# Kernel optimization log

Hardware: AMD Instinct MI355X
Metric: run time of the kernel (lower is better)

## Reference

```python
import jax, jax.numpy as jnp
import numpy as np

N = 50000      # nodes
E = 800000     # edges (avg degree 16)
D = 64         # input_dim
L = 64         # latent_dim


def setup_inputs() -> dict:
    key = jax.random.key(0)
    k1, k2, k3, k4, k5, k6 = jax.random.split(key, 6)
    x = jax.random.normal(k1, (N, D), dtype=jnp.float32)
    weight = jax.random.normal(k2, (D, L), dtype=jnp.float32) / np.sqrt(D)
    bias = jax.random.normal(k3, (L,), dtype=jnp.float32) * 0.01
    # strictly positive degrees to keep division well-behaved
    node_degree = jax.random.uniform(k4, (N, 1), dtype=jnp.float32) + 1.0
    edge_src = jax.random.randint(k5, (E,), 0, N, dtype=jnp.int32)
    edge_dst = jax.random.randint(k6, (E,), 0, N, dtype=jnp.int32)
    return {"x": x, "weight": weight, "bias": bias,
            "node_degree": node_degree,
            "edge_src": edge_src, "edge_dst": edge_dst}


def reference(x, weight, bias, node_degree, edge_src, edge_dst):
    # gnn_spmm(adj, x): sparse aggregate over incoming edges -> [N, D]
    agg = jax.ops.segment_sum(x[edge_src], edge_dst, num_segments=N)
    pooled = agg + x                      # residual self-connection
    node_linear = pooled @ weight + bias  # dense projection [N, L]
    normalized = node_linear / node_degree  # normalize_embedding == 2
    return jax.nn.relu(normalized)
```

## Files before the change

kernel.cpp:

```cpp
#include <hip/hip_runtime.h>
#include <hip/hip_fp16.h>

#define N_NODES 50000
#define DIM 64
#define CB 782
#define CAP 1280
#define EPT 12
#define EB (512 * EPT)
#define BINCAP 64
#define ZROW N_NODES

typedef _Float16 half8 __attribute__((ext_vector_type(8)));
typedef float floatx4 __attribute__((ext_vector_type(4)));

#define WS_CURSOR  0
#define WS_COARSE  4096
#define WS_YH      (WS_COARSE + 4003840)

__global__ void __launch_bounds__(512) prep_kernel(
        const float* __restrict__ x, const float* __restrict__ W,
        const int* __restrict__ edge_src, const int* __restrict__ edge_dst,
        int* __restrict__ cursor, unsigned int* __restrict__ coarse,
        _Float16* __restrict__ yh, int E, int pa) {
    int b = blockIdx.x, t = threadIdx.x;
    if (b < pa) {
        __shared__ int lhist[CB];
        __shared__ int lbase[CB];
        for (int i = t; i < CB; i += 512) lhist[i] = 0;
        __syncthreads();

        int base = b * EB;
        unsigned int pk[EPT];
        int bk[EPT];
        #pragma unroll
        for (int jj = 0; jj < EPT / 4; ++jj) {
            int e4 = base + jj * 2048 + t * 4;
            if (e4 + 3 < E) {
                int4 s4 = *reinterpret_cast<const int4*>(edge_src + e4);
                int4 d4 = *reinterpret_cast<const int4*>(edge_dst + e4);
                int ss[4] = {s4.x, s4.y, s4.z, s4.w};
                int dd[4] = {d4.x, d4.y, d4.z, d4.w};
                #pragma unroll
                for (int u = 0; u < 4; ++u) {
                    int j = jj * 4 + u;
                    bk[j] = dd[u] >> 6;
                    pk[j] = ((unsigned int)ss[u] << 6) | (unsigned int)(dd[u] & 63);
                    atomicAdd(&lhist[bk[j]], 1);
                }
            } else {
                #pragma unroll
                for (int u = 0; u < 4; ++u) {
                    int j = jj * 4 + u;
                    int e = e4 + u;
                    bk[j] = -1;
                    if (e < E) {
                        int s = edge_src[e];
                        int d = edge_dst[e];
                        bk[j] = d >> 6;
                        pk[j] = ((unsigned int)s << 6) | (unsigned int)(d & 63);
                        atomicAdd(&lhist[bk[j]], 1);
                    }
                }
            }
        }
        __syncthreads();
        for (int i = t; i < CB; i += 512) {
            lbase[i] = atomicAdd(&cursor[i], lhist[i]);
            lhist[i] = 0;
        }
        __syncthreads();
        #pragma unroll
        for (int j = 0; j < EPT; ++j) {
            if (bk[j] >= 0) {
                int r = atomicAdd(&lhist[bk[j]], 1);
                coarse[(size_t)bk[j] * CAP + lbase[bk[j]] + r] = pk[j];
            }
        }
    } else {
        __shared__ _Float16 wh[64 * 80];
        #pragma unroll
        for (int i = 0; i < 8; ++i) {
            int idx = i * 512 + t;
            int k = idx >> 6, n = idx & 63;
            wh[n * 80 + k] = (_Float16)W[idx];
        }
        __syncthreads();

        int wv = t >> 6, lane = t & 63;
        int m = lane & 15, q = lane >> 4;
        int rbase = (b - pa) * 128 + wv * 16;
        int row = rbase + m;
        int rowc = row < N_NODES ? row : N_NODES - 1;
        const float* xp = x + (size_t)rowc * DIM + q * 8;
        float4 f0 = *reinterpret_cast<const float4*>(xp);
        float4 f1 = *reinterpret_cast<const float4*>(xp + 4);
        float4 f2 = *reinterpret_cast<const float4*>(xp + 32);
        float4 f3 = *reinterpret_cast<const float4*>(xp + 36);
        half8 a0 = {(_Float16)f0.x, (_Float16)f0.y, (_Float16)f0.z, (_Float16)f0.w,
                    (_Float16)f1.x, (_Float16)f1.y, (_Float16)f1.z, (_Float16)f1.w};
        half8 a1 = {(_Float16)f2.x, (_Float16)f2.y, (_Float16)f2.z, (_Float16)f2.w,
                    (_Float16)f3.x, (_Float16)f3.y, (_Float16)f3.z, (_Float16)f3.w};

        floatx4 accp[4];
        #pragma unroll
        for (int tt = 0; tt < 4; ++tt) {
            half8 bb0 = *reinterpret_cast<const half8*>(&wh[(tt * 16 + m) * 80 + q * 8]);
            half8 bb1 = *reinterpret_cast<const half8*>(&wh[(tt * 16 + m) * 80 + 32 + q * 8]);
            floatx4 cf = {0.f, 0.f, 0.f, 0.f};
            cf = __builtin_amdgcn_mfma_f32_16x16x32_f16(a0, bb0, cf, 0, 0, 0);
            cf = __builtin_amdgcn_mfma_f32_16x16x32_f16(a1, bb1, cf, 0, 0, 0);
            accp[tt] = cf;
        }
        #pragma unroll
        for (int r = 0; r < 4; ++r) {
            int orow = rbase + q * 4 + r;
            if (orow < N_NODES) {
                #pragma unroll
                for (int tt = 0; tt < 4; ++tt)
                    yh[(size_t)orow * DIM + tt * 16 + m] = (_Float16)accp[tt][r];
            } else {
                #pragma unroll
                for (int tt = 0; tt < 4; ++tt)
                    yh[(size_t)orow * DIM + tt * 16 + m] = (_Float16)0.f;
            }
        }
    }
}

__global__ void __launch_bounds__(512, 6) fused_kernel(
        const _Float16* __restrict__ yh,
        const float* __restrict__ bias,
        const float* __restrict__ deg,
        const int* __restrict__ cursor,
        const unsigned int* __restrict__ coarse,
        float* __restrict__ out) {
    __shared__ int sedges[64 * BINCAP];
    __shared__ int cur[64];

    int t = threadIdx.x;
    int b = blockIdx.x;
    int nb = b * 64;
    int cnt = cursor[b];
    const unsigned int* cbk = coarse + (size_t)b * CAP;

    if (t < 64) cur[t] = 0;
    __syncthreads();

    for (int i = t; i < cnt; i += 512) {
        unsigned int e = cbk[i];
        int bin = (int)(e & 63u);
        int p = atomicAdd(&cur[bin], 1);
        sedges[bin * BINCAP + p] = (int)(e >> 6);
    }
    __syncthreads();

    int g = t >> 3;
    int c = t & 7;

    {
        int cc = cur[g];
        int s = cc + c;
        if (s < ((cc + 7) & ~7) && s < BINCAP)
            sedges[g * BINCAP + s] = ZROW;
    }
    __syncthreads();

    int node = nb + g;

    float bj[8];
    *reinterpret_cast<float4*>(&bj[0]) = reinterpret_cast<const float4*>(bias)[c * 2];
    *reinterpret_cast<float4*>(&bj[4]) = reinterpret_cast<const float4*>(bias)[c * 2 + 1];

    float acc[8];
    #pragma unroll
    for (int j = 0; j < 8; ++j) acc[j] = 0.f;
    const int* bp = &sedges[g * BINCAP];
    int ct8 = (cur[g] + 7) & ~7;
    for (int k = 0; k < ct8; k += 8) {
        int4 sa = *reinterpret_cast<const int4*>(bp + k);
        int4 sb = *reinterpret_cast<const int4*>(bp + k + 4);
        int sid[8] = {sa.x, sa.y, sa.z, sa.w, sb.x, sb.y, sb.z, sb.w};
        half8 v[8];
        #pragma unroll
        for (int u = 0; u < 8; ++u)
            v[u] = *reinterpret_cast<const half8*>(yh + (size_t)sid[u] * DIM + c * 8);
        half8 s0 = v[0] + v[1];
        half8 s1 = v[2] + v[3];
        half8 s2 = v[4] + v[5];
        half8 s3 = v[6] + v[7];
        half8 u0 = s0 + s1;
        half8 u1 = s2 + s3;
        half8 w  = u0 + u1;
        #pragma unroll
        for (int j = 0; j < 8; ++j) acc[j] += (float)w[j];
    }

    if (node < N_NODES) {
        half8 r = *reinterpret_cast<const half8*>(yh + (size_t)node * DIM + c * 8);
        float inv = 1.0f / deg[node];
        float o[8];
        #pragma unroll
        for (int j = 0; j < 8; ++j)
            o[j] = fmaxf((acc[j] + (float)r[j] + bj[j]) * inv, 0.f);
        float4* op = reinterpret_cast<float4*>(out + (size_t)node * DIM + c * 8);
        op[0] = make_float4(o[0], o[1], o[2], o[3]);
        op[1] = make_float4(o[4], o[5], o[6], o[7]);
    }
}

extern "C" void kernel_launch(void* const* d_in, const int* in_sizes, int n_in,
                              void* d_out, int out_size, void* d_ws, size_t ws_size,
                              hipStream_t stream) {
    const float* x        = (const float*)d_in[0];
    const float* weight   = (const float*)d_in[1];
    const float* bias     = (const float*)d_in[2];
    const float* node_deg = (const float*)d_in[3];
    const int*   edge_src = (const int*)d_in[4];
    const int*   edge_dst = (const int*)d_in[5];
    float* out = (float*)d_out;
    const int E = in_sizes[4];

    char* ws = (char*)d_ws;
    int*          cursor = (int*)(ws + WS_CURSOR);
    unsigned int* coarse = (unsigned int*)(ws + WS_COARSE);
    _Float16*     yh     = (_Float16*)(ws + WS_YH);

    hipMemsetAsync(cursor, 0, CB * sizeof(int), stream);

    int pa = (E + EB - 1) / EB;
    prep_kernel<<<pa + 391, 512, 0, stream>>>(
        x, weight, edge_src, edge_dst, cursor, coarse, yh, E, pa);

    fused_kernel<<<CB, 512, 0, stream>>>(
        yh, bias, node_deg, cursor, coarse, out);
}
```

Before: 103.3 us.

## Halve nodes per block and split each row across sixteen lanes

```diff
diff --git a/kernel.cpp b/kernel.cpp
--- a/kernel.cpp
+++ b/kernel.cpp
@@ -3,19 +3,20 @@
 
 #define N_NODES 50000
 #define DIM 64
-#define CB 782
-#define CAP 1280
+#define CB 1563
+#define CAP 640
 #define EPT 12
 #define EB (512 * EPT)
 #define BINCAP 64
 #define ZROW N_NODES
 
 typedef _Float16 half8 __attribute__((ext_vector_type(8)));
+typedef _Float16 half4v __attribute__((ext_vector_type(4)));
 typedef float floatx4 __attribute__((ext_vector_type(4)));
 
 #define WS_CURSOR  0
-#define WS_COARSE  4096
-#define WS_YH      (WS_COARSE + 4003840)
+#define WS_COARSE  8192
+#define WS_YH      (WS_COARSE + 4001280)
 
 __global__ void __launch_bounds__(512) prep_kernel(
         const float* __restrict__ x, const float* __restrict__ W,
@@ -43,8 +44,8 @@
                 #pragma unroll
                 for (int u = 0; u < 4; ++u) {
                     int j = jj * 4 + u;
-                    bk[j] = dd[u] >> 6;
-                    pk[j] = ((unsigned int)ss[u] << 6) | (unsigned int)(dd[u] & 63);
+                    bk[j] = dd[u] >> 5;
+                    pk[j] = ((unsigned int)ss[u] << 5) | (unsigned int)(dd[u] & 31);
                     atomicAdd(&lhist[bk[j]], 1);
                 }
             } else {
@@ -56,8 +57,8 @@
                     if (e < E) {
                         int s = edge_src[e];
                         int d = edge_dst[e];
-                        bk[j] = d >> 6;
-                        pk[j] = ((unsigned int)s << 6) | (unsigned int)(d & 63);
+                        bk[j] = d >> 5;
+                        pk[j] = ((unsigned int)s << 5) | (unsigned int)(d & 31);
                         atomicAdd(&lhist[bk[j]], 1);
                     }
                 }
@@ -127,35 +128,35 @@
     }
 }
 
-__global__ void __launch_bounds__(512, 6) fused_kernel(
+__global__ void __launch_bounds__(512, 8) fused_kernel(
         const _Float16* __restrict__ yh,
         const float* __restrict__ bias,
         const float* __restrict__ deg,
         const int* __restrict__ cursor,
         const unsigned int* __restrict__ coarse,
         float* __restrict__ out) {
-    __shared__ int sedges[64 * BINCAP];
-    __shared__ int cur[64];
+    __shared__ int sedges[32 * BINCAP];
+    __shared__ int cur[32];
 
     int t = threadIdx.x;
     int b = blockIdx.x;
-    int nb = b * 64;
+    int nb = b * 32;
     int cnt = cursor[b];
     const unsigned int* cbk = coarse + (size_t)b * CAP;
 
-    if (t < 64) cur[t] = 0;
+    if (t < 32) cur[t] = 0;
     __syncthreads();
 
     for (int i = t; i < cnt; i += 512) {
         unsigned int e = cbk[i];
-        int bin = (int)(e & 63u);
+        int bin = (int)(e & 31u);
         int p = atomicAdd(&cur[bin], 1);
-        sedges[bin * BINCAP + p] = (int)(e >> 6);
+        sedges[bin * BINCAP + p] = (int)(e >> 5);
     }
     __syncthreads();
 
-    int g = t >> 3;
-    int c = t & 7;
+    int g = t >> 4;
+    int c = t & 15;
 
     {
         int cc = cur[g];
@@ -167,44 +168,41 @@
 
     int node = nb + g;
 
-    float bj[8];
-    *reinterpret_cast<float4*>(&bj[0]) = reinterpret_cast<const float4*>(bias)[c * 2];
-    *reinterpret_cast<float4*>(&bj[4]) = reinterpret_cast<const float4*>(bias)[c * 2 + 1];
-
-    float acc[8];
+    float4 bj = reinterpret_cast<const float4*>(bias)[c];
+
+    float acc[4];
     #pragma unroll
-    for (int j = 0; j < 8; ++j) acc[j] = 0.f;
+    for (int j = 0; j < 4; ++j) acc[j] = 0.f;
     const int* bp = &sedges[g * BINCAP];
     int ct8 = (cur[g] + 7) & ~7;
     for (int k = 0; k < ct8; k += 8) {
         int4 sa = *reinterpret_cast<const int4*>(bp + k);
         int4 sb = *reinterpret_cast<const int4*>(bp + k + 4);
         int sid[8] = {sa.x, sa.y, sa.z, sa.w, sb.x, sb.y, sb.z, sb.w};
-        half8 v[8];
+        half4v v[8];
         #pragma unroll
         for (int u = 0; u < 8; ++u)
-            v[u] = *reinterpret_cast<const half8*>(yh + (size_t)sid[u] * DIM + c * 8);
-        half8 s0 = v[0] + v[1];
-        half8 s1 = v[2] + v[3];
-        half8 s2 = v[4] + v[5];
-        half8 s3 = v[6] + v[7];
-        half8 u0 = s0 + s1;
-        half8 u1 = s2 + s3;
-        half8 w  = u0 + u1;
-        #pragma unroll
-        for (int j = 0; j < 8; ++j) acc[j] += (float)w[j];
+            v[u] = *reinterpret_cast<const half4v*>(yh + (size_t)sid[u] * DIM + c * 4);
+        half4v s0 = v[0] + v[1];
+        half4v s1 = v[2] + v[3];
+        half4v s2 = v[4] + v[5];
+        half4v s3 = v[6] + v[7];
+        half4v u0 = s0 + s1;
+        half4v u1 = s2 + s3;
+        half4v w  = u0 + u1;
+        #pragma unroll
+        for (int j = 0; j < 4; ++j) acc[j] += (float)w[j];
     }
 
     if (node < N_NODES) {
-        half8 r = *reinterpret_cast<const half8*>(yh + (size_t)node * DIM + c * 8);
+        half4v r = *reinterpret_cast<const half4v*>(yh + (size_t)node * DIM + c * 4);
         float inv = 1.0f / deg[node];
-        float o[8];
-        #pragma unroll
-        for (int j = 0; j < 8; ++j)
-            o[j] = fmaxf((acc[j] + (float)r[j] + bj[j]) * inv, 0.f);
-        float4* op = reinterpret_cast<float4*>(out + (size_t)node * DIM + c * 8);
-        op[0] = make_float4(o[0], o[1], o[2], o[3]);
-        op[1] = make_float4(o[4], o[5], o[6], o[7]);
+        float4 o;
+        o.x = fmaxf((acc[0] + (float)r[0] + bj.x) * inv, 0.f);
+        o.y = fmaxf((acc[1] + (float)r[1] + bj.y) * inv, 0.f);
+        o.z = fmaxf((acc[2] + (float)r[2] + bj.z) * inv, 0.f);
+        o.w = fmaxf((acc[3] + (float)r[3] + bj.w) * inv, 0.f);
+        *reinterpret_cast<float4*>(out + (size_t)node * DIM + c * 4) = o;
     }
 }
 
```

After: 104.5 us. About the same (+1.2%).
